# Kernel optimization log

Hardware: AMD Instinct MI355X
Metric: run time of the kernel (lower is better)

## Reference

```python
import jax, jax.numpy as jnp
import numpy as np


def setup_inputs() -> dict:
    key = jax.random.key(0)
    k1, k2, k3 = jax.random.split(key, 3)
    N, C, S = 8192, 256, 7
    D = C * S * S            # 12544 flattened RoI feature dim
    NUM_CLASSES = 81         # includes background (softmax cls head)
    x = jax.random.normal(k1, (N, C, S, S), dtype=jnp.float32)
    # fc weights ~ N(0, 0.01) like mmdet's normal init
    W_cls = jax.random.normal(k2, (NUM_CLASSES, D), dtype=jnp.float32) * 0.01
    b_cls = jnp.zeros((NUM_CLASSES,), dtype=jnp.float32)
    W_reg = jax.random.normal(k3, (4 * NUM_CLASSES, D), dtype=jnp.float32) * 0.001
    b_reg = jnp.zeros((4 * NUM_CLASSES,), dtype=jnp.float32)
    return {"x": x, "W_cls": W_cls, "b_cls": b_cls, "W_reg": W_reg, "b_reg": b_reg}


def reference(x, W_cls, b_cls, W_reg, b_reg):
    # BBoxHead.forward: flatten RoI features, then cls / reg FC heads.
    N = x.shape[0]
    feat = x.reshape(N, -1)                      # [N, C*S*S]
    cls_score = feat @ W_cls.T + b_cls           # [N, num_classes]
    bbox_pred = feat @ W_reg.T + b_reg           # [N, 4*num_classes]
    return cls_score, bbox_pred
```

## Files before the change

### kernel.cpp

```cpp
#include <hip/hip_runtime.h>
#include <stdint.h>
#include <stddef.h>

#define K_FULL 12544
#define M_ROWS 8192
#define NCLS 81
#define NREG 324
#define NTOT 405
#define NPAD 416
#define OUT0 663552
#define OUT_TOTAL 3317760

typedef __bf16 bf16x8 __attribute__((ext_vector_type(8)));
typedef float floatx4 __attribute__((ext_vector_type(4)));

__device__ __forceinline__ uint32_t pack2_bf16(float a, float b) {
  uint32_t ua = __float_as_uint(a);
  uint32_t ub = __float_as_uint(b);
  ua = (ua + 0x7FFFu + ((ua >> 16) & 1u)) >> 16;
  ub = (ub + 0x7FFFu + ((ub >> 16) & 1u)) >> 16;
  return ua | (ub << 16);
}

__global__ void pack_w(const float* __restrict__ Wc, const float* __restrict__ Wr,
                       uint16_t* __restrict__ Wb) {
  const int u = blockIdx.x * blockDim.x + threadIdx.x;
  if (u >= (K_FULL / 8)) return;
  const int row = blockIdx.y;
  uint4 v = {0u, 0u, 0u, 0u};
  const float* src = nullptr;
  if (row < NCLS) src = Wc + (size_t)row * K_FULL;
  else if (row < NTOT) src = Wr + (size_t)(row - NCLS) * K_FULL;
  if (src) {
    const float4 f0 = *(const float4*)(src + u * 8);
    const float4 f1 = *(const float4*)(src + u * 8 + 4);
    v.x = pack2_bf16(f0.x, f0.y);
    v.y = pack2_bf16(f0.z, f0.w);
    v.z = pack2_bf16(f1.x, f1.y);
    v.w = pack2_bf16(f1.z, f1.w);
  }
  *(uint4*)(Wb + (size_t)row * K_FULL + u * 8) = v;
}

__global__ void bias_init(const float* __restrict__ bc, const float* __restrict__ br,
                          float* __restrict__ out) {
  const int i = blockIdx.x * blockDim.x + threadIdx.x;
  if (i >= OUT_TOTAL) return;
  if (i < OUT0) {
    out[i] = bc[i % NCLS];
  } else {
    const int j = i - OUT0;
    out[i] = br[j % NREG];
  }
}

__global__ __launch_bounds__(256, 2) void gemm_kernel(
    const float* __restrict__ x, const uint16_t* __restrict__ Wb,
    float* __restrict__ out) {
  __shared__ uint4 sA4[512];
  __shared__ uint4 sB4[3328];
  uint8_t* sA = (uint8_t*)sA4;
  uint8_t* sB = (uint8_t*)sB4;

  const int tid = threadIdx.x;
  const int lane = tid & 63;
  const int wave = tid >> 6;
  const int mg = wave >> 1;
  const int ng = wave & 1;

  const int mt = blockIdx.x >> 2;
  const int ks = blockIdx.x & 3;
  const int rowBase = mt * 64;
  int k0 = ks * 3136;
  const int kEnd = k0 + 3136;

  floatx4 acc[2][13];
  const floatx4 zero = {0.0f, 0.0f, 0.0f, 0.0f};
#pragma unroll
  for (int i = 0; i < 2; ++i)
#pragma unroll
    for (int j = 0; j < 13; ++j) acc[i][j] = zero;

  const int rA = tid >> 3;
  const int pA = tid & 7;
  const int kA = pA ^ (rA & 7);
  const float* gA0 = x + (size_t)(rowBase + rA) * K_FULL + k0 + kA * 8;
  const float* gA1 = gA0 + (size_t)32 * K_FULL;

  const int rB = lane >> 3;
  const int pB = lane & 7;
  const int kbB = pB ^ rB;

  float4 pf0 = *(const float4*)gA0;
  float4 pf1 = *(const float4*)(gA0 + 4);
  float4 pf2 = *(const float4*)gA1;
  float4 pf3 = *(const float4*)(gA1 + 4);
  gA0 += 64;
  gA1 += 64;

  for (; k0 < kEnd; k0 += 64) {
    __syncthreads();

    {
      uint4 v;
      v.x = pack2_bf16(pf0.x, pf0.y);
      v.y = pack2_bf16(pf0.z, pf0.w);
      v.z = pack2_bf16(pf1.x, pf1.y);
      v.w = pack2_bf16(pf1.z, pf1.w);
      *(uint4*)(sA + rA * 128 + pA * 16) = v;
      uint4 w;
      w.x = pack2_bf16(pf2.x, pf2.y);
      w.y = pack2_bf16(pf2.z, pf2.w);
      w.z = pack2_bf16(pf3.x, pf3.y);
      w.w = pack2_bf16(pf3.z, pf3.w);
      *(uint4*)(sA + (rA + 32) * 128 + pA * 16) = w;
    }

    for (int i = wave; i < 52; i += 4) {
      const int n = i * 8 + rB;
      const uint16_t* g = Wb + (size_t)n * K_FULL + (k0 + kbB * 8);
      __builtin_amdgcn_global_load_lds(
          (const __attribute__((address_space(1))) void*)g,
          (__attribute__((address_space(3))) void*)(sB + i * 1024), 16, 0, 0);
    }

    __syncthreads();

    if (k0 + 64 < kEnd) {
      pf0 = *(const float4*)gA0;
      pf1 = *(const float4*)(gA0 + 4);
      pf2 = *(const float4*)gA1;
      pf3 = *(const float4*)(gA1 + 4);
      gA0 += 64;
      gA1 += 64;
    }

    const int q = lane >> 4;
    const int c0 = lane & 15;
    const int m0 = mg * 32 + c0;
#pragma unroll
    for (int s = 0; s < 2; ++s) {
      const int kb = s * 4 + q;
      const int ksw = (kb ^ (m0 & 7)) * 16;
      const bf16x8 a0 = *(const bf16x8*)(sA + m0 * 128 + ksw);
      const bf16x8 a1 = *(const bf16x8*)(sA + (m0 + 16) * 128 + ksw);
#pragma unroll
      for (int nf = 0; nf < 13; ++nf) {
        const int n = ng * 208 + nf * 16 + c0;
        const bf16x8 b = *(const bf16x8*)(sB + n * 128 + ((kb ^ (n & 7)) * 16));
        acc[0][nf] = __builtin_amdgcn_mfma_f32_16x16x32_bf16(a0, b, acc[0][nf], 0, 0, 0);
        acc[1][nf] = __builtin_amdgcn_mfma_f32_16x16x32_bf16(a1, b, acc[1][nf], 0, 0, 0);
      }
    }
  }

  const int q = lane >> 4;
  const int c0 = lane & 15;
#pragma unroll
  for (int i = 0; i < 2; ++i) {
    const int r0 = rowBase + mg * 32 + i * 16 + q * 4;
#pragma unroll
    for (int nf = 0; nf < 13; ++nf) {
      const int col = ng * 208 + nf * 16 + c0;
      if (col < NCLS) {
        float* dst = out + (size_t)r0 * NCLS + col;
#pragma unroll
        for (int r = 0; r < 4; ++r)
          unsafeAtomicAdd(dst + (size_t)r * NCLS, acc[i][nf][r]);
      } else if (col < NTOT) {
        float* dst = out + OUT0 + (size_t)r0 * NREG + (col - NCLS);
#pragma unroll
        for (int r = 0; r < 4; ++r)
          unsafeAtomicAdd(dst + (size_t)r * NREG, acc[i][nf][r]);
      }
    }
  }
}

extern "C" void kernel_launch(void* const* d_in, const int* in_sizes, int n_in,
                              void* d_out, int out_size, void* d_ws, size_t ws_size,
                              hipStream_t stream) {
  const float* x = (const float*)d_in[0];
  const float* Wc = (const float*)d_in[1];
  const float* bc = (const float*)d_in[2];
  const float* Wr = (const float*)d_in[3];
  const float* br = (const float*)d_in[4];
  float* out = (float*)d_out;
  uint16_t* Wb = (uint16_t*)d_ws;

  pack_w<<<dim3(7, 416), dim3(256), 0, stream>>>(Wc, Wr, Wb);
  bias_init<<<dim3((OUT_TOTAL + 255) / 256), dim3(256), 0, stream>>>(bc, br, out);
  gemm_kernel<<<dim3(512), dim3(256), 0, stream>>>(x, Wb, out);
}
```

Measured before the change: 661.4 us.

## Double-buffer weight tiles in LDS and double rows per block

The GEMM block grows to 512 threads covering 128 rows instead of 64, halving the grid. The weight tile is now double-buffered in LDS: the next k-chunk's global-to-LDS loads are issued before computing on the current buffer, so weight fetch overlaps MFMA work. Each weight tile is reused across twice as many rows, cutting weight traffic. The cost is about 122KB of LDS per block, which likely allows only one block per CU, and fewer blocks overall.

```diff
diff --git a/kernel.cpp b/kernel.cpp
--- a/kernel.cpp
+++ b/kernel.cpp
@@ -54,13 +54,14 @@
   }
 }
 
-__global__ __launch_bounds__(256, 2) void gemm_kernel(
+__global__ __launch_bounds__(512, 2) void gemm_kernel(
     const float* __restrict__ x, const uint16_t* __restrict__ Wb,
     float* __restrict__ out) {
-  __shared__ uint4 sA4[512];
-  __shared__ uint4 sB4[3328];
+  __shared__ uint4 sA4[1024];
+  __shared__ uint4 sB4[2][3328];
   uint8_t* sA = (uint8_t*)sA4;
-  uint8_t* sB = (uint8_t*)sB4;
+  uint8_t* sBcur = (uint8_t*)sB4[0];
+  uint8_t* sBnext = (uint8_t*)sB4[1];
 
   const int tid = threadIdx.x;
   const int lane = tid & 63;
@@ -70,9 +71,8 @@
 
   const int mt = blockIdx.x >> 2;
   const int ks = blockIdx.x & 3;
-  const int rowBase = mt * 64;
-  int k0 = ks * 3136;
-  const int kEnd = k0 + 3136;
+  const int rowBase = mt * 128;
+  const int kBase = ks * 3136;
 
   floatx4 acc[2][13];
   const floatx4 zero = {0.0f, 0.0f, 0.0f, 0.0f};
@@ -84,13 +84,19 @@
   const int rA = tid >> 3;
   const int pA = tid & 7;
   const int kA = pA ^ (rA & 7);
-  const float* gA0 = x + (size_t)(rowBase + rA) * K_FULL + k0 + kA * 8;
-  const float* gA1 = gA0 + (size_t)32 * K_FULL;
+  const float* gA0 = x + (size_t)(rowBase + rA) * K_FULL + kBase + kA * 8;
+  const float* gA1 = gA0 + (size_t)64 * K_FULL;
 
   const int rB = lane >> 3;
   const int pB = lane & 7;
   const int kbB = pB ^ rB;
 
+  for (int i = wave; i < 52; i += 8) {
+    const uint16_t* g = Wb + (size_t)(i * 8 + rB) * K_FULL + (kBase + kbB * 8);
+    __builtin_amdgcn_global_load_lds(
+        (const __attribute__((address_space(1))) void*)g,
+        (__attribute__((address_space(3))) void*)(sBcur + i * 1024), 16, 0, 0);
+  }
   float4 pf0 = *(const float4*)gA0;
   float4 pf1 = *(const float4*)(gA0 + 4);
   float4 pf2 = *(const float4*)gA1;
@@ -98,7 +104,7 @@
   gA0 += 64;
   gA1 += 64;
 
-  for (; k0 < kEnd; k0 += 64) {
+  for (int c = 0; c < 49; ++c) {
     __syncthreads();
 
     {
@@ -113,20 +119,19 @@
       w.y = pack2_bf16(pf2.z, pf2.w);
       w.z = pack2_bf16(pf3.x, pf3.y);
       w.w = pack2_bf16(pf3.z, pf3.w);
-      *(uint4*)(sA + (rA + 32) * 128 + pA * 16) = w;
-    }
-
-    for (int i = wave; i < 52; i += 4) {
-      const int n = i * 8 + rB;
-      const uint16_t* g = Wb + (size_t)n * K_FULL + (k0 + kbB * 8);
-      __builtin_amdgcn_global_load_lds(
-          (const __attribute__((address_space(1))) void*)g,
-          (__attribute__((address_space(3))) void*)(sB + i * 1024), 16, 0, 0);
+      *(uint4*)(sA + (rA + 64) * 128 + pA * 16) = w;
     }
 
     __syncthreads();
 
-    if (k0 + 64 < kEnd) {
+    if (c + 1 < 49) {
+      const int kNext = kBase + (c + 1) * 64;
+      for (int i = wave; i < 52; i += 8) {
+        const uint16_t* g = Wb + (size_t)(i * 8 + rB) * K_FULL + (kNext + kbB * 8);
+        __builtin_amdgcn_global_load_lds(
+            (const __attribute__((address_space(1))) void*)g,
+            (__attribute__((address_space(3))) void*)(sBnext + i * 1024), 16, 0, 0);
+      }
       pf0 = *(const float4*)gA0;
       pf1 = *(const float4*)(gA0 + 4);
       pf2 = *(const float4*)gA1;
@@ -147,11 +152,15 @@
 #pragma unroll
       for (int nf = 0; nf < 13; ++nf) {
         const int n = ng * 208 + nf * 16 + c0;
-        const bf16x8 b = *(const bf16x8*)(sB + n * 128 + ((kb ^ (n & 7)) * 16));
+        const bf16x8 b = *(const bf16x8*)(sBcur + n * 128 + ((kb ^ (n & 7)) * 16));
         acc[0][nf] = __builtin_amdgcn_mfma_f32_16x16x32_bf16(a0, b, acc[0][nf], 0, 0, 0);
         acc[1][nf] = __builtin_amdgcn_mfma_f32_16x16x32_bf16(a1, b, acc[1][nf], 0, 0, 0);
       }
     }
+
+    uint8_t* t = sBcur;
+    sBcur = sBnext;
+    sBnext = t;
   }
 
   const int q = lane >> 4;
@@ -190,5 +199,5 @@
 
   pack_w<<<dim3(7, 416), dim3(256), 0, stream>>>(Wc, Wr, Wb);
   bias_init<<<dim3((OUT_TOTAL + 255) / 256), dim3(256), 0, stream>>>(bc, br, out);
-  gemm_kernel<<<dim3(512), dim3(256), 0, stream>>>(x, Wb, out);
-}
+  gemm_kernel<<<dim3(256), dim3(512), 0, stream>>>(x, Wb, out);
+}
```

Result: no change. 665.4 us (+0.6%).
